# Kernel optimization log

Measured on AMD Instinct MI355X. Metric: run time of the kernel, lower is better.

The kernel has to match this reference:

```python
import jax, jax.numpy as jnp
import numpy as np
from jax import lax

WS = (4, 8, 8)        # window_size (D,H,W)
DIM = 128
HEADS = 4
HD = DIM // HEADS      # 32
SCALE = HD ** -0.5     # swinv1, lif neuron -> head_dim**-0.5
TAU = 2.0
VTH = 1.0
ALPHA = 2.0            # ATan surrogate width


def _rel_pos_index(ws):
    # static numpy computation of relative_position_index, shape (N, N)
    coords = np.stack(np.meshgrid(np.arange(ws[0]), np.arange(ws[1]), np.arange(ws[2]), indexing='ij'))
    cf = coords.reshape(3, -1)                      # (3, N)
    rel = (cf[:, :, None] - cf[:, None, :]).transpose(1, 2, 0).astype(np.int64)  # (N,N,3)
    rel[:, :, 0] += ws[0] - 1
    rel[:, :, 1] += ws[1] - 1
    rel[:, :, 2] += ws[2] - 1
    rel[:, :, 0] *= (2 * ws[1] - 1) * (2 * ws[2] - 1)
    rel[:, :, 1] *= 2 * ws[2] - 1
    return rel.sum(-1)

RPI = _rel_pos_index(WS)  # (N, N) int


@jax.custom_vjp
def spike(x):
    return (x >= 0.0).astype(x.dtype)

def _spike_fwd(x):
    return spike(x), x

def _spike_bwd(x, g):
    # ATan surrogate gradient (spikingjelly default)
    return (g * (ALPHA / (2.0 * (1.0 + (np.pi / 2.0 * ALPHA * x) ** 2))),)

spike.defvjp(_spike_fwd, _spike_bwd)


def lif(x):
    # multi-step LIF over leading time axis: v' = v + (x - v)/tau, hard reset to 0
    def step(v, xt):
        v = v + (xt - v) / TAU
        s = spike(v - VTH)
        return v * (1.0 - s), s
    return lax.scan(step, jnp.zeros_like(x[0]), x)[1]


def setup_inputs() -> dict:
    key = jax.random.key(0)
    ks = jax.random.split(key, 7)
    x = jax.random.normal(ks[0], (WS[0], 256, WS[1], WS[2], DIM), dtype=jnp.float32)
    Wq = jax.random.normal(ks[1], (DIM, DIM), dtype=jnp.float32) * 0.02
    Wk = jax.random.normal(ks[2], (DIM, DIM), dtype=jnp.float32) * 0.02
    Wv = jax.random.normal(ks[3], (DIM, DIM), dtype=jnp.float32) * 0.02
    rpb_table = jax.random.normal(ks[4], ((2 * WS[0] - 1) * (2 * WS[1] - 1) * (2 * WS[2] - 1), HEADS), dtype=jnp.float32) * 0.02
    Wproj = jax.random.normal(ks[5], (DIM, DIM), dtype=jnp.float32) * 0.02
    bproj = jax.random.normal(ks[6], (DIM,), dtype=jnp.float32) * 0.02
    return {"x": x, "Wq": Wq, "Wk": Wk, "Wv": Wv, "rpb_table": rpb_table, "Wproj": Wproj, "bproj": bproj}


def reference(x, Wq, Wk, Wv, rpb_table, Wproj, bproj):
    T, B_, H, W, C = x.shape
    N = T * H * W
    # QKV: linear (no bias) -> spiking neuron over time axis
    q = lif(jnp.einsum('tbhwc,dc->tbhwd', x, Wq))
    k = lif(jnp.einsum('tbhwc,dc->tbhwd', x, Wk))
    v = lif(jnp.einsum('tbhwc,dc->tbhwd', x, Wv))
    # literal row-major reshape as in torch: (T,B_,H,W,C) -> (B_, heads, N, hd)
    q = q.reshape(B_, HEADS, N, HD)
    k = k.reshape(B_, HEADS, N, HD)
    v = v.reshape(B_, HEADS, N, HD)
    # scaled QK^T (NO softmax in the original forward)
    attn = jnp.einsum('bhnd,bhmd->bhnm', q * SCALE, k)
    rpb = rpb_table[RPI.reshape(-1)].reshape(N, N, HEADS).transpose(2, 0, 1)  # (heads,N,N)
    attn = attn + rpb[None]
    out = jnp.einsum('bhnm,bhmd->bhnd', attn, v)
    out = out.reshape(B_, HEADS, T, H, W, HD).transpose(2, 0, 3, 4, 1, 5).reshape(T, B_, H, W, C)
    out = jnp.einsum('tbhwc,dc->tbhwd', out, Wproj) + bproj
    out = lif(out).reshape(B_, N, C)
    return (out, attn)
```

## Files before the change

### kernel.cpp

```cpp
#include <hip/hip_runtime.h>
#include <hip/hip_bf16.h>


typedef __attribute__((ext_vector_type(8))) short bf16x8;
typedef __attribute__((ext_vector_type(4))) float f32x4;

#define MFMA16(a, b, c) __builtin_amdgcn_mfma_f32_16x16x32_bf16((a), (b), (c), 0, 0, 0)

#define BAR_LDS()                                                \
    do {                                                         \
        asm volatile("s_waitcnt lgkmcnt(0)" ::: "memory");       \
        __builtin_amdgcn_s_barrier();                            \
    } while (0)

__device__ __forceinline__ unsigned short f2bf(float f) {
    union { __hip_bfloat16 h; unsigned short u; } cv;
    cv.h = __float2bfloat16(f);
    return cv.u;
}

__device__ __forceinline__ void cvt8_store_reg(unsigned short* dst, float4 f0, float4 f1) {
    unsigned short h[8];
    h[0] = f2bf(f0.x); h[1] = f2bf(f0.y); h[2] = f2bf(f0.z); h[3] = f2bf(f0.w);
    h[4] = f2bf(f1.x); h[5] = f2bf(f1.y); h[6] = f2bf(f1.z); h[7] = f2bf(f1.w);
    *(uint4*)dst = *(const uint4*)h;
}

__device__ __forceinline__ void cvt8_store(unsigned short* dst, const float* src) {
    float4 f0 = *(const float4*)(src);
    float4 f1 = *(const float4*)(src + 4);
    cvt8_store_reg(dst, f0, f1);
}

__global__ __launch_bounds__(256) void k_qkv_lif(
    const float* __restrict__ x,
    const float* __restrict__ Wq,
    const float* __restrict__ Wk,
    const float* __restrict__ Wv,
    unsigned int* __restrict__ qbits,
    unsigned int* __restrict__ kbits,
    unsigned int* __restrict__ vbits)
{
    __shared__ unsigned short Wl[128 * 136];
    __shared__ unsigned short Xl[64 * 136];

    const int tid = threadIdx.x;
    const int wv = tid >> 6, lane = tid & 63;
    const int l15 = lane & 15, lh = lane >> 4;
    const int wsel = blockIdx.y;
    const float* W = (wsel == 0) ? Wq : (wsel == 1) ? Wk : Wv;
    unsigned int* bits = (wsel == 0) ? qbits : (wsel == 1) ? kbits : vbits;
    const int B = blockIdx.x;

    {
#pragma unroll
        for (int i = 0; i < 8; ++i) {
            int e = i * 2048 + tid * 8;
            cvt8_store(&Wl[(e >> 7) * 136 + (e & 127)], W + e);
        }
    }

    float4 px[8];
    {
        const float* xg = x + B * 8192;
#pragma unroll
        for (int i = 0; i < 4; ++i) {
            int e = i * 2048 + tid * 8;
            px[2 * i]     = *(const float4*)(xg + e);
            px[2 * i + 1] = *(const float4*)(xg + e + 4);
        }
    }

    f32x4 vst[8];
#pragma unroll
    for (int nt = 0; nt < 8; ++nt) vst[nt] = (f32x4){0.f, 0.f, 0.f, 0.f};

    for (int t = 0; t < 4; ++t) {
        BAR_LDS();
#pragma unroll
        for (int i = 0; i < 4; ++i) {
            int e = i * 2048 + tid * 8;
            cvt8_store_reg(&Xl[(e >> 7) * 136 + (e & 127)], px[2 * i], px[2 * i + 1]);
        }
        BAR_LDS();

        if (t < 3) {
            const float* xg = x + (t + 1) * 2097152 + B * 8192;
#pragma unroll
            for (int i = 0; i < 4; ++i) {
                int e = i * 2048 + tid * 8;
                px[2 * i]     = *(const float4*)(xg + e);
                px[2 * i + 1] = *(const float4*)(xg + e + 4);
            }
        }

        f32x4 acc[8];
#pragma unroll
        for (int nt = 0; nt < 8; ++nt) acc[nt] = (f32x4){0.f, 0.f, 0.f, 0.f};
#pragma unroll
        for (int kk = 0; kk < 4; ++kk) {
            bf16x8 a = *(const bf16x8*)&Xl[(wv * 16 + l15) * 136 + kk * 32 + lh * 8];
#pragma unroll
            for (int nt = 0; nt < 8; ++nt) {
                bf16x8 b = *(const bf16x8*)&Wl[(nt * 16 + l15) * 136 + kk * 32 + lh * 8];
                acc[nt] = MFMA16(a, b, acc[nt]);
            }
        }
        unsigned short sp[8][4];
#pragma unroll
        for (int nt = 0; nt < 8; ++nt) {
#pragma unroll
            for (int reg = 0; reg < 4; ++reg) {
                float y = acc[nt][reg];
                float v = vst[nt][reg];
                v = v + (y - v) * 0.5f;
                float s = (v >= 1.0f) ? 1.0f : 0.0f;
                vst[nt][reg] = v * (1.0f - s);
                sp[nt][reg] = (s != 0.0f) ? (unsigned short)1 : (unsigned short)0;
            }
        }
        BAR_LDS();
#pragma unroll
        for (int nt = 0; nt < 8; ++nt)
#pragma unroll
            for (int reg = 0; reg < 4; ++reg)
                Xl[(wv * 16 + lh * 4 + reg) * 136 + nt * 16 + l15] = sp[nt][reg];
        BAR_LDS();
        {
            const unsigned short* rowp = &Xl[(tid >> 2) * 136 + (tid & 3) * 32];
            unsigned int mask = 0;
#pragma unroll
            for (int j8 = 0; j8 < 4; ++j8) {
                uint4 u = *(const uint4*)(rowp + j8 * 8);
                int base = j8 * 8;
                if (u.x & 0xFFFFu) mask |= 1u << (base + 0);
                if (u.x >> 16)     mask |= 1u << (base + 1);
                if (u.y & 0xFFFFu) mask |= 1u << (base + 2);
                if (u.y >> 16)     mask |= 1u << (base + 3);
                if (u.z & 0xFFFFu) mask |= 1u << (base + 4);
                if (u.z >> 16)     mask |= 1u << (base + 5);
                if (u.w & 0xFFFFu) mask |= 1u << (base + 6);
                if (u.w >> 16)     mask |= 1u << (base + 7);
            }
            bits[(t * 256 + B) * 256 + tid] = mask;
        }
    }
}

__global__ __launch_bounds__(256) void k_attn(
    const unsigned int* __restrict__ qbits,
    const unsigned int* __restrict__ kbits,
    const unsigned int* __restrict__ vbits,
    const float* __restrict__ tbl,
    float* __restrict__ attn_out,
    unsigned short* __restrict__ o_ws)
{
    __shared__ unsigned short vT[32 * 264];
    __shared__ unsigned short attnL[32 * 264];
    __shared__ float tblL[1575];

    const int tid = threadIdx.x;
    const int wv = tid >> 6, lane = tid & 63;
    const int l15 = lane & 15, lh = lane >> 4;
    const int g = blockIdx.x, hh = g & 3;

    for (int i = tid; i < 1575; i += 256)
        tblL[i] = tbl[i * 4 + hh];

    uint4 km = *(const uint4*)&kbits[g * 256 + (tid & 63) * 4];
    {
        unsigned int vb = vbits[g * 256 + tid];
#pragma unroll
        for (int d = 0; d < 32; ++d)
            vT[d * 264 + tid] = ((vb >> d) & 1u) ? (unsigned short)0x3F80
                                                 : (unsigned short)0;
    }

    const int m0 = (tid & 63) * 4;
    int dm[4];
#pragma unroll
    for (int i = 0; i < 4; ++i) {
        int m = m0 + i;
        dm[i] = (m >> 6) * 225 + ((m >> 3) & 7) * 15 + (m & 7);
    }

    BAR_LDS();

    const float SC = 0.17677669529663687f;
    float* attn_b = attn_out + (size_t)g * 65536;
    unsigned short* ob = o_ws + g * 8192;
    const int rowb = __builtin_amdgcn_readfirstlane(wv * 8);
    const int rt = wv >> 1, nh = wv & 1;

    for (int c = 0; c < 8; ++c) {
#pragma unroll
        for (int j = 0; j < 8; ++j) {
            int n = c * 32 + rowb + j;
            unsigned int qn = qbits[g * 256 + n];
            int zn = n >> 6, yn = (n >> 3) & 7, xn = n & 7;
            int basei = zn * 225 + yn * 15 + xn + 787;
            f32x4 av;
            av.x = (float)__popc(qn & km.x) * SC + tblL[basei - dm[0]];
            av.y = (float)__popc(qn & km.y) * SC + tblL[basei - dm[1]];
            av.z = (float)__popc(qn & km.z) * SC + tblL[basei - dm[2]];
            av.w = (float)__popc(qn & km.w) * SC + tblL[basei - dm[3]];
            __builtin_nontemporal_store(av, (f32x4*)(attn_b + n * 256 + m0));
            unsigned int p0 = (unsigned int)f2bf(av.x) | ((unsigned int)f2bf(av.y) << 16);
            unsigned int p1 = (unsigned int)f2bf(av.z) | ((unsigned int)f2bf(av.w) << 16);
            uint2 pk; pk.x = p0; pk.y = p1;
            *(uint2*)&attnL[(rowb + j) * 264 + m0] = pk;
        }
        BAR_LDS();
        f32x4 oc = (f32x4){0.f, 0.f, 0.f, 0.f};
#pragma unroll
        for (int kk = 0; kk < 8; ++kk) {
            bf16x8 a = *(const bf16x8*)&attnL[(rt * 16 + l15) * 264 + kk * 32 + lh * 8];
            bf16x8 b = *(const bf16x8*)&vT[(nh * 16 + l15) * 264 + kk * 32 + lh * 8];
            oc = MFMA16(a, b, oc);
        }
#pragma unroll
        for (int reg = 0; reg < 4; ++reg) {
            int n = c * 32 + rt * 16 + lh * 4 + reg;
            ob[n * 32 + nh * 16 + l15] = f2bf(oc[reg]);
        }
        BAR_LDS();
    }
}

__global__ __launch_bounds__(256) void k_proj_lif(
    const unsigned short* __restrict__ o_ws,
    const float* __restrict__ Wp,
    const float* __restrict__ bp,
    float* __restrict__ out0)
{
    __shared__ unsigned short Wl[128 * 136];
    __shared__ unsigned short Al[64 * 136];

    const int tid = threadIdx.x;
    const int wv = tid >> 6, lane = tid & 63;
    const int l15 = lane & 15, lh = lane >> 4;
    const int b = blockIdx.x >> 1, half = blockIdx.x & 1;

    {
#pragma unroll
        for (int i = 0; i < 8; ++i) {
            int e = i * 2048 + tid * 8;
            cvt8_store(&Wl[(e >> 7) * 136 + (e & 127)], Wp + e);
        }
    }

    float biasf[2];
#pragma unroll
    for (int ntl = 0; ntl < 2; ++ntl)
        biasf[ntl] = bp[(wv * 2 + ntl) * 16 + l15];

    const unsigned short* ob = o_ws + b * 32768;

    uint4 pa[4];
    {
        int c = half * 2;
#pragma unroll
        for (int i = 0; i < 4; ++i) {
            int e = i * 2048 + tid * 8;
            int lr2 = e >> 7, cc = e & 127;
            int t2 = lr2 >> 4, rit = lr2 & 15;
            int n = t2 * 64 + c * 16 + rit;
            pa[i] = *(const uint4*)(ob + (((cc >> 5) * 256 + n) * 32) + (cc & 31));
        }
    }

    for (int ci = 0; ci < 2; ++ci) {
        const int c = half * 2 + ci;
        BAR_LDS();
#pragma unroll
        for (int i = 0; i < 4; ++i) {
            int e = i * 2048 + tid * 8;
            *(uint4*)&Al[(e >> 7) * 136 + (e & 127)] = pa[i];
        }
        BAR_LDS();

        if (ci == 0) {
            int c1 = c + 1;
#pragma unroll
            for (int i = 0; i < 4; ++i) {
                int e = i * 2048 + tid * 8;
                int lr2 = e >> 7, cc = e & 127;
                int t2 = lr2 >> 4, rit = lr2 & 15;
                int n = t2 * 64 + c1 * 16 + rit;
                pa[i] = *(const uint4*)(ob + (((cc >> 5) * 256 + n) * 32) + (cc & 31));
            }
        }

        f32x4 acc[4][2];
#pragma unroll
        for (int t2 = 0; t2 < 4; ++t2)
#pragma unroll
            for (int ntl = 0; ntl < 2; ++ntl)
                acc[t2][ntl] = (f32x4){0.f, 0.f, 0.f, 0.f};
#pragma unroll
        for (int kk = 0; kk < 4; ++kk) {
            bf16x8 a[4];
#pragma unroll
            for (int t2 = 0; t2 < 4; ++t2)
                a[t2] = *(const bf16x8*)&Al[(t2 * 16 + l15) * 136 + kk * 32 + lh * 8];
#pragma unroll
            for (int ntl = 0; ntl < 2; ++ntl) {
                bf16x8 bb = *(const bf16x8*)&Wl[((wv * 2 + ntl) * 16 + l15) * 136 + kk * 32 + lh * 8];
#pragma unroll
                for (int t2 = 0; t2 < 4; ++t2)
                    acc[t2][ntl] = MFMA16(a[t2], bb, acc[t2][ntl]);
            }
        }
#pragma unroll
        for (int ntl = 0; ntl < 2; ++ntl) {
            int d = (wv * 2 + ntl) * 16 + l15;
#pragma unroll
            for (int reg = 0; reg < 4; ++reg) {
                int hw = c * 16 + lh * 4 + reg;
                float v = 0.f;
#pragma unroll
                for (int t2 = 0; t2 < 4; ++t2) {
                    float y = acc[t2][ntl][reg] + biasf[ntl];
                    v = v + (y - v) * 0.5f;
                    float s = (v >= 1.0f) ? 1.0f : 0.0f;
                    v = v * (1.0f - s);
                    __builtin_nontemporal_store(
                        s, out0 + t2 * 2097152 + b * 8192 + hw * 128 + d);
                }
            }
        }
    }
}

extern "C" void kernel_launch(void* const* d_in, const int* in_sizes, int n_in,
                              void* d_out, int out_size, void* d_ws, size_t ws_size,
                              hipStream_t stream)
{
    const float* x   = (const float*)d_in[0];
    const float* Wq  = (const float*)d_in[1];
    const float* Wk  = (const float*)d_in[2];
    const float* Wv  = (const float*)d_in[3];
    const float* tbl = (const float*)d_in[4];
    const float* Wp  = (const float*)d_in[5];
    const float* bp  = (const float*)d_in[6];

    float* out0 = (float*)d_out;
    float* attn = out0 + 8388608;

    unsigned short* o_ws = (unsigned short*)d_ws;
    unsigned int* qbits = (unsigned int*)(o_ws + 8388608);
    unsigned int* kbits = qbits + 262144;
    unsigned int* vbits = kbits + 262144;

    k_qkv_lif<<<dim3(256, 3), 256, 0, stream>>>(x, Wq, Wk, Wv,
                                                qbits, kbits, vbits);
    k_attn<<<1024, 256, 0, stream>>>(qbits, kbits, vbits, tbl, attn, o_ws);
    k_proj_lif<<<512, 256, 0, stream>>>(o_ws, Wp, bp, out0);
}
```

Baseline: 356.4 us.

## Give each wave private attention rows to drop block barriers in attn kernel

Result: no change. 354.3 us (-0.6%).

```diff
diff --git a/kernel.cpp b/kernel.cpp
--- a/kernel.cpp
+++ b/kernel.cpp
@@ -11,6 +11,12 @@
     do {                                                         \
         asm volatile("s_waitcnt lgkmcnt(0)" ::: "memory");       \
         __builtin_amdgcn_s_barrier();                            \
+    } while (0)
+
+#define FENCE_LDS_WAVE()                                         \
+    do {                                                         \
+        asm volatile("s_waitcnt lgkmcnt(0)" ::: "memory");       \
+        __builtin_amdgcn_sched_barrier(0);                       \
     } while (0)
 
 __device__ __forceinline__ unsigned short f2bf(float f) {
@@ -156,7 +162,7 @@
     unsigned short* __restrict__ o_ws)
 {
     __shared__ unsigned short vT[32 * 264];
-    __shared__ unsigned short attnL[32 * 264];
+    __shared__ unsigned short attnW[4][16 * 260];
     __shared__ float tblL[1575];
 
     const int tid = threadIdx.x;
@@ -167,7 +173,7 @@
     for (int i = tid; i < 1575; i += 256)
         tblL[i] = tbl[i * 4 + hh];
 
-    uint4 km = *(const uint4*)&kbits[g * 256 + (tid & 63) * 4];
+    uint4 km = *(const uint4*)&kbits[g * 256 + lane * 4];
     {
         unsigned int vb = vbits[g * 256 + tid];
 #pragma unroll
@@ -176,7 +182,7 @@
                                                  : (unsigned short)0;
     }
 
-    const int m0 = (tid & 63) * 4;
+    const int m0 = lane * 4;
     int dm[4];
 #pragma unroll
     for (int i = 0; i < 4; ++i) {
@@ -189,13 +195,13 @@
     const float SC = 0.17677669529663687f;
     float* attn_b = attn_out + (size_t)g * 65536;
     unsigned short* ob = o_ws + g * 8192;
-    const int rowb = __builtin_amdgcn_readfirstlane(wv * 8);
-    const int rt = wv >> 1, nh = wv & 1;
-
-    for (int c = 0; c < 8; ++c) {
-#pragma unroll
-        for (int j = 0; j < 8; ++j) {
-            int n = c * 32 + rowb + j;
+    const int nb = __builtin_amdgcn_readfirstlane(wv * 64);
+    unsigned short* aw = &attnW[wv][0];
+
+    for (int rt = 0; rt < 4; ++rt) {
+#pragma unroll
+        for (int j = 0; j < 16; ++j) {
+            int n = nb + rt * 16 + j;
             unsigned int qn = qbits[g * 256 + n];
             int zn = n >> 6, yn = (n >> 3) & 7, xn = n & 7;
             int basei = zn * 225 + yn * 15 + xn + 787;
@@ -208,22 +214,26 @@
             unsigned int p0 = (unsigned int)f2bf(av.x) | ((unsigned int)f2bf(av.y) << 16);
             unsigned int p1 = (unsigned int)f2bf(av.z) | ((unsigned int)f2bf(av.w) << 16);
             uint2 pk; pk.x = p0; pk.y = p1;
-            *(uint2*)&attnL[(rowb + j) * 264 + m0] = pk;
-        }
-        BAR_LDS();
-        f32x4 oc = (f32x4){0.f, 0.f, 0.f, 0.f};
+            *(uint2*)&aw[j * 260 + m0] = pk;
+        }
+        FENCE_LDS_WAVE();
+
+        f32x4 oc0 = (f32x4){0.f, 0.f, 0.f, 0.f};
+        f32x4 oc1 = (f32x4){0.f, 0.f, 0.f, 0.f};
 #pragma unroll
         for (int kk = 0; kk < 8; ++kk) {
-            bf16x8 a = *(const bf16x8*)&attnL[(rt * 16 + l15) * 264 + kk * 32 + lh * 8];
-            bf16x8 b = *(const bf16x8*)&vT[(nh * 16 + l15) * 264 + kk * 32 + lh * 8];
-            oc = MFMA16(a, b, oc);
+            bf16x8 a  = *(const bf16x8*)&aw[l15 * 260 + kk * 32 + lh * 8];
+            bf16x8 b0 = *(const bf16x8*)&vT[l15 * 264 + kk * 32 + lh * 8];
+            bf16x8 b1 = *(const bf16x8*)&vT[(16 + l15) * 264 + kk * 32 + lh * 8];
+            oc0 = MFMA16(a, b0, oc0);
+            oc1 = MFMA16(a, b1, oc1);
         }
 #pragma unroll
         for (int reg = 0; reg < 4; ++reg) {
-            int n = c * 32 + rt * 16 + lh * 4 + reg;
-            ob[n * 32 + nh * 16 + l15] = f2bf(oc[reg]);
-        }
-        BAR_LDS();
+            int n = nb + rt * 16 + lh * 4 + reg;
+            ob[n * 32 + l15]      = f2bf(oc0[reg]);
+            ob[n * 32 + 16 + l15] = f2bf(oc1[reg]);
+        }
     }
 }
 
```
